# Optimization experiments

Hardware: AMD Instinct MI355X
Metric: run time of the kernel (lower is better)

The kernel has to match this reference:

```python
import jax, jax.numpy as jnp
import numpy as np
from jax.scipy.linalg import expm

A = 4
D = 8
WIDTH = 16
V = 1024
S = 1024
C = 4
T_INF = 1000.0


def setup_inputs() -> dict:
    key = jax.random.key(0)
    ks = jax.random.split(key, 8)
    return {
        "embeddings_VxD": jax.random.normal(ks[0], (V, D), dtype=jnp.float32),
        "site_positions_SxC": jax.random.uniform(ks[1], (S, C), dtype=jnp.float32),
        "W0": jax.random.normal(ks[2], (D, WIDTH), dtype=jnp.float32) * (1.0 / np.sqrt(D)),
        "b0": jnp.zeros((WIDTH,), dtype=jnp.float32),
        "W1": jax.random.normal(ks[3], (WIDTH, WIDTH), dtype=jnp.float32) * (1.0 / np.sqrt(WIDTH)),
        "b1": jnp.zeros((WIDTH,), dtype=jnp.float32),
        "Wout": jax.random.normal(ks[4], (WIDTH, A * A), dtype=jnp.float32) * (1.0 / np.sqrt(WIDTH)),
        "bout": jnp.zeros((A * A,), dtype=jnp.float32),
    }


def _q_matrix(emb_VxD, W0, b0, W1, b1, Wout, bout):
    # MLP: D -> width -> width -> A*A (ReLU hidden layers, depth=2)
    h = jax.nn.relu(emb_VxD @ W0 + b0)
    h = jax.nn.relu(h @ W1 + b1)
    log_q_VxAA = h @ Wout + bout                      # [V, A*A]
    Q = jnp.exp(log_q_VxAA.reshape(-1, A, A))         # [V, A, A]
    diag = jnp.eye(A, dtype=bool)
    Q = jnp.where(diag, 0.0, Q)                        # zero diagonal
    Q = Q / jnp.sum(Q, axis=-1, keepdims=True)         # row-normalize off-diagonal
    Q = jnp.where(diag, -1.0, Q)                       # diagonal = -1 (rows sum to 0)
    return Q


def reference(embeddings_VxD, site_positions_SxC, W0, b0, W1, b1, Wout, bout):
    Q_VxAxA = _q_matrix(embeddings_VxD, W0, b0, W1, b1, Wout, bout)
    S_ = site_positions_SxC.shape[0]
    V_ = Q_VxAxA.shape[0]
    # Q matrix is identical across sites; original expands to [V,S,A,A] and
    # applies matrix_exp per (v,s) pair.
    Q_VSxAxA = jnp.broadcast_to(Q_VxAxA[:, None] * T_INF, (V_, S_, A, A)).reshape(-1, A, A)
    expm_VSxAxA = jax.vmap(expm)(Q_VSxAxA)
    stat_probs_VxSxA = expm_VSxAxA.reshape(V_, S_, A, A)[:, :, 0]  # first row = stationary probs
    return stat_probs_VxSxA
```

## Files before the change

### kernel.cpp

```cpp
#include <hip/hip_runtime.h>
#include <math.h>


namespace {

constexpr int kA = 4;
constexpr int kD = 8;
constexpr int kW = 16;
constexpr int kV = 1024;
constexpr int kS = 1024;
constexpr int kSquarings = 14;
constexpr int kTaylorOrder = 8;

__device__ inline double det3(double m00, double m01, double m02,
                              double m10, double m11, double m12,
                              double m20, double m21, double m22) {
  return m00 * (m11 * m22 - m12 * m21) -
         m01 * (m10 * m22 - m12 * m20) +
         m02 * (m10 * m21 - m11 * m20);
}

__global__ __launch_bounds__(64) void fused_kernel(
    const float* __restrict__ emb,
    const float* __restrict__ W0,
    const float* __restrict__ b0,
    const float* __restrict__ W1,
    const float* __restrict__ b1,
    const float* __restrict__ Wout,
    const float* __restrict__ bout,
    float4* __restrict__ out) {
  const int v = blockIdx.x;

  float x[kD];
#pragma unroll
  for (int d = 0; d < kD; ++d) x[d] = emb[v * kD + d];

  float h0[kW];
#pragma unroll
  for (int j = 0; j < kW; ++j) {
    float acc = b0[j];
#pragma unroll
    for (int d = 0; d < kD; ++d) acc = fmaf(x[d], W0[d * kW + j], acc);
    h0[j] = fmaxf(acc, 0.0f);
  }

  float h1[kW];
#pragma unroll
  for (int j = 0; j < kW; ++j) {
    float acc = b1[j];
#pragma unroll
    for (int k = 0; k < kW; ++k) acc = fmaf(h0[k], W1[k * kW + j], acc);
    h1[j] = fmaxf(acc, 0.0f);
  }

  float l[kA * kA];
#pragma unroll
  for (int j = 0; j < kA * kA; ++j) {
    float acc = bout[j];
#pragma unroll
    for (int k = 0; k < kW; ++k)
      acc = fmaf(h1[k], Wout[k * (kA * kA) + j], acc);
    l[j] = acc;
  }

  double Q[kA][kA];
#pragma unroll
  for (int i = 0; i < kA; ++i) {
    float m = -3.0e38f;
#pragma unroll
    for (int j = 0; j < kA; ++j)
      if (j != i) m = fmaxf(m, l[i * kA + j]);
    float e[kA];
    float ssumf = 0.0f;
#pragma unroll
    for (int j = 0; j < kA; ++j) {
      e[j] = (j == i) ? 0.0f : __expf(l[i * kA + j] - m);
      ssumf += e[j];
    }
    const float inv = 1.0f / ssumf;
#pragma unroll
    for (int j = 0; j < kA; ++j)
      Q[i][j] = (j == i) ? -1.0 : (double)(e[j] * inv);
  }

  const double c0 = det3(Q[1][1], Q[1][2], Q[1][3],
                         Q[2][1], Q[2][2], Q[2][3],
                         Q[3][1], Q[3][2], Q[3][3]);
  const double c1 = det3(Q[0][0], Q[0][2], Q[0][3],
                         Q[2][0], Q[2][2], Q[2][3],
                         Q[3][0], Q[3][2], Q[3][3]);
  const double c2 = det3(Q[0][0], Q[0][1], Q[0][3],
                         Q[1][0], Q[1][1], Q[1][3],
                         Q[3][0], Q[3][1], Q[3][3]);
  const double c3 = det3(Q[0][0], Q[0][1], Q[0][2],
                         Q[1][0], Q[1][1], Q[1][2],
                         Q[2][0], Q[2][1], Q[2][2]);
  const double csum = c0 + c1 + c2 + c3;

  double s2 = 0.0;
#pragma unroll
  for (int i = 0; i < kA; ++i)
#pragma unroll
    for (int j = i + 1; j < kA; ++j) s2 = fma(Q[i][j], Q[j][i], s2);
  const double e2 = 6.0 - s2;

  constexpr double dlt = 0.03;
  const double a0 = -csum;
  const double a2s = 4.0 - 3.0 * dlt;
  const double a1s = e2 - 8.0 * dlt + 3.0 * dlt * dlt;
  const double a0s = a0 - e2 * dlt + 4.0 * dlt * dlt - dlt * dlt * dlt;
  const bool fast = (a1s > 0.0) && (a0s > 0.0) && (a2s * a1s > a0s);

  float4 rvec;
  if (fast) {
    const double inv = 1.0 / csum;
    rvec = make_float4((float)(c0 * inv), (float)(c1 * inv),
                       (float)(c2 * inv), (float)(c3 * inv));
  } else {
    const double tau = 1000.0 / (double)(1 << kSquarings);
    double M[kA][kA];
#pragma unroll
    for (int i = 0; i < kA; ++i)
#pragma unroll
      for (int j = 0; j < kA; ++j) M[i][j] = tau * Q[i][j];

    double T[kA][kA];
#pragma unroll
    for (int i = 0; i < kA; ++i)
#pragma unroll
      for (int j = 0; j < kA; ++j) T[i][j] = (i == j) ? 1.0 : 0.0;

#pragma unroll 1
    for (int k = kTaylorOrder; k >= 1; --k) {
      double U[kA][kA];
#pragma unroll
      for (int i = 0; i < kA; ++i)
#pragma unroll
        for (int j = 0; j < kA; ++j) {
          double acc = 0.0;
#pragma unroll
          for (int p = 0; p < kA; ++p) acc = fma(M[i][p], T[p][j], acc);
          U[i][j] = acc;
        }
      const double rk = 1.0 / (double)k;
#pragma unroll
      for (int i = 0; i < kA; ++i)
#pragma unroll
        for (int j = 0; j < kA; ++j)
          T[i][j] = ((i == j) ? 1.0 : 0.0) + U[i][j] * rk;
    }

#pragma unroll 1
    for (int t = 0; t < kSquarings - 1; ++t) {
      double U[kA][kA];
#pragma unroll
      for (int i = 0; i < kA; ++i)
#pragma unroll
        for (int j = 0; j < kA; ++j) {
          double acc = 0.0;
#pragma unroll
          for (int p = 0; p < kA; ++p) acc = fma(T[i][p], T[p][j], acc);
          U[i][j] = acc;
        }
#pragma unroll
      for (int i = 0; i < kA; ++i)
#pragma unroll
        for (int j = 0; j < kA; ++j) T[i][j] = U[i][j];
    }

    double r0[kA];
#pragma unroll
    for (int j = 0; j < kA; ++j) {
      double acc = 0.0;
#pragma unroll
      for (int p = 0; p < kA; ++p) acc = fma(T[0][p], T[p][j], acc);
      r0[j] = acc;
    }
    rvec = make_float4((float)r0[0], (float)r0[1], (float)r0[2], (float)r0[3]);
  }

  float4* o = out + (size_t)v * kS;
#pragma unroll
  for (int k = 0; k < kS / 64; ++k) o[k * 64 + threadIdx.x] = rvec;
}

}

extern "C" void kernel_launch(void* const* d_in, const int* in_sizes, int n_in,
                              void* d_out, int out_size, void* d_ws,
                              size_t ws_size, hipStream_t stream) {
  const float* emb  = (const float*)d_in[0];
  const float* W0   = (const float*)d_in[2];
  const float* b0   = (const float*)d_in[3];
  const float* W1   = (const float*)d_in[4];
  const float* b1   = (const float*)d_in[5];
  const float* Wout = (const float*)d_in[6];
  const float* bout = (const float*)d_in[7];

  fused_kernel<<<kV, 64, 0, stream>>>(emb, W0, b0, W1, b1, Wout, bout,
                                      (float4*)d_out);
}
```

Baseline: 12.38 us.

## Distribute MLP neurons across lanes with shuffles instead of redundant per-thread compute

Each of the first 16 lanes of the block now computes one hidden unit and one output logit, using column-cached weights, and exchanges activations with wavefront shuffles. Before, every thread recomputed the whole MLP serially. Row softmax normalization uses xor shuffles, and the 4x4 Q matrix is gathered to all lanes by broadcast shuffles. This cuts the serial FMA chain and the redundant weight loads per thread. It drops the max-subtraction before exp, which risks overflow for large logits, and it adds shuffle latency.

```diff
diff --git a/kernel.cpp b/kernel.cpp
--- a/kernel.cpp
+++ b/kernel.cpp
@@ -30,58 +30,52 @@
     const float* __restrict__ bout,
     float4* __restrict__ out) {
   const int v = blockIdx.x;
+  const int lane = threadIdx.x;
+  const int n = lane & 15;
+
+  float w0c[kD];
+#pragma unroll
+  for (int d = 0; d < kD; ++d) w0c[d] = W0[d * kW + n];
+  float w1c[kW];
+#pragma unroll
+  for (int k = 0; k < kW; ++k) w1c[k] = W1[k * kW + n];
+  float woc[kW];
+#pragma unroll
+  for (int k = 0; k < kW; ++k) woc[k] = Wout[k * (kA * kA) + n];
+  const float b0n = b0[n];
+  const float b1n = b1[n];
+  const float botn = bout[n];
 
   float x[kD];
 #pragma unroll
   for (int d = 0; d < kD; ++d) x[d] = emb[v * kD + d];
 
-  float h0[kW];
+  float acc = b0n;
 #pragma unroll
-  for (int j = 0; j < kW; ++j) {
-    float acc = b0[j];
+  for (int d = 0; d < kD; ++d) acc = fmaf(x[d], w0c[d], acc);
+  const float h0 = fmaxf(acc, 0.0f);
+
+  acc = b1n;
 #pragma unroll
-    for (int d = 0; d < kD; ++d) acc = fmaf(x[d], W0[d * kW + j], acc);
-    h0[j] = fmaxf(acc, 0.0f);
-  }
+  for (int k = 0; k < kW; ++k) acc = fmaf(__shfl(h0, k), w1c[k], acc);
+  const float h1 = fmaxf(acc, 0.0f);
 
-  float h1[kW];
+  acc = botn;
 #pragma unroll
-  for (int j = 0; j < kW; ++j) {
-    float acc = b1[j];
-#pragma unroll
-    for (int k = 0; k < kW; ++k) acc = fmaf(h0[k], W1[k * kW + j], acc);
-    h1[j] = fmaxf(acc, 0.0f);
-  }
+  for (int k = 0; k < kW; ++k) acc = fmaf(__shfl(h1, k), woc[k], acc);
+  const float ln = acc;
 
-  float l[kA * kA];
-#pragma unroll
-  for (int j = 0; j < kA * kA; ++j) {
-    float acc = bout[j];
-#pragma unroll
-    for (int k = 0; k < kW; ++k)
-      acc = fmaf(h1[k], Wout[k * (kA * kA) + j], acc);
-    l[j] = acc;
-  }
+  const int ri = n >> 2, cj = n & 3;
+  const float e = (ri == cj) ? 0.0f : __expf(ln);
+  float s = e + __shfl_xor(e, 1);
+  s = s + __shfl_xor(s, 2);
+  const float qf = e * (1.0f / s);
 
   double Q[kA][kA];
 #pragma unroll
-  for (int i = 0; i < kA; ++i) {
-    float m = -3.0e38f;
+  for (int m = 0; m < kA * kA; ++m) Q[m >> 2][m & 3] = (double)__shfl(qf, m);
 #pragma unroll
-    for (int j = 0; j < kA; ++j)
-      if (j != i) m = fmaxf(m, l[i * kA + j]);
-    float e[kA];
-    float ssumf = 0.0f;
-#pragma unroll
-    for (int j = 0; j < kA; ++j) {
-      e[j] = (j == i) ? 0.0f : __expf(l[i * kA + j] - m);
-      ssumf += e[j];
-    }
-    const float inv = 1.0f / ssumf;
-#pragma unroll
-    for (int j = 0; j < kA; ++j)
-      Q[i][j] = (j == i) ? -1.0 : (double)(e[j] * inv);
-  }
+  for (int i = 0; i < kA; ++i) Q[i][i] = -1.0;
 
   const double c0 = det3(Q[1][1], Q[1][2], Q[1][3],
                          Q[2][1], Q[2][2], Q[2][3],
@@ -137,10 +131,10 @@
       for (int i = 0; i < kA; ++i)
 #pragma unroll
         for (int j = 0; j < kA; ++j) {
-          double acc = 0.0;
+          double a = 0.0;
 #pragma unroll
-          for (int p = 0; p < kA; ++p) acc = fma(M[i][p], T[p][j], acc);
-          U[i][j] = acc;
+          for (int p = 0; p < kA; ++p) a = fma(M[i][p], T[p][j], a);
+          U[i][j] = a;
         }
       const double rk = 1.0 / (double)k;
 #pragma unroll
@@ -157,10 +151,10 @@
       for (int i = 0; i < kA; ++i)
 #pragma unroll
         for (int j = 0; j < kA; ++j) {
-          double acc = 0.0;
+          double a = 0.0;
 #pragma unroll
-          for (int p = 0; p < kA; ++p) acc = fma(T[i][p], T[p][j], acc);
-          U[i][j] = acc;
+          for (int p = 0; p < kA; ++p) a = fma(T[i][p], T[p][j], a);
+          U[i][j] = a;
         }
 #pragma unroll
       for (int i = 0; i < kA; ++i)
@@ -171,10 +165,10 @@
     double r0[kA];
 #pragma unroll
     for (int j = 0; j < kA; ++j) {
-      double acc = 0.0;
+      double a = 0.0;
 #pragma unroll
-      for (int p = 0; p < kA; ++p) acc = fma(T[0][p], T[p][j], acc);
-      r0[j] = acc;
+      for (int p = 0; p < kA; ++p) a = fma(T[0][p], T[p][j], a);
+      r0[j] = a;
     }
     rvec = make_float4((float)r0[0], (float)r0[1], (float)r0[2], (float)r0[3]);
   }
```

Result: faster. 11.40 us (-7.9%).
